# Kernel tuning notes

Hardware: AMD Instinct MI355X
Metric: run time of the kernel (lower is better)

## Reference

```python
import jax, jax.numpy as jnp
import numpy as np

ALPHA, GAMMA = 0.25, 2.0
ACCEPT, REJECT = 0.5, 0.4
CLF_W, REG_W = 1.0, 50.0
SL1_R = 9.0  # reg_smooth_l1_loss_scaling_factor
EPS = 1e-4


def _calc_iou(a, b):
    # a: [A,4] anchors in yxyx ; b: [M,4] gt boxes in xyxy (as in original code)
    ay1, ax1, ay2, ax2 = a[:, 0], a[:, 1], a[:, 2], a[:, 3]
    bx1, by1, bx2, by2 = b[:, 0], b[:, 1], b[:, 2], b[:, 3]
    iw = jnp.clip(jnp.minimum(ax2[:, None], bx2) - jnp.maximum(ax1[:, None], bx1), 0.0)
    ih = jnp.clip(jnp.minimum(ay2[:, None], by2) - jnp.maximum(ay1[:, None], by1), 0.0)
    inter = iw * ih  # [A, M]
    aarea = ((ax2 - ax1) * (ay2 - ay1))[:, None]
    barea = (bx2 - bx1) * (by2 - by1)
    union = jnp.clip(aarea + barea - inter, 1e-8)
    return inter / union


def _single_image(clf, reg, ann, anchors, a_cx, a_cy, a_w, a_h):
    # clf: [A,C], reg: [A,4], ann: [M,5] (x1,y1,x2,y2,label; label=-1 => pad)
    clf = jnp.clip(clf, EPS, 1.0 - EPS)
    labels = ann[:, 4]
    valid = labels != -1.0  # [M]
    boxes = ann[:, :4]
    iou = _calc_iou(anchors, boxes)               # [A, M]
    iou = jnp.where(valid[None, :], iou, -1.0)    # invalid GT never matches
    iou_max = iou.max(axis=-1)                    # [A]
    iou_arg = iou.argmax(axis=-1)                 # [A]
    matched = iou_max > ACCEPT
    unmatched = iou_max < REJECT
    num_matched = matched.sum()
    # classification targets: -1 (ignore) by default, 0 for unmatched, one-hot for matched
    gt_lbl = labels[iou_arg].astype(jnp.int32) - 1  # [A]
    one_hot = jax.nn.one_hot(gt_lbl, clf.shape[-1], dtype=clf.dtype)
    tgt = jnp.where(matched[:, None], one_hot,
                    jnp.where(unmatched[:, None], 0.0, -1.0))
    pos = ALPHA * (1.0 - clf) ** GAMMA * (-jnp.log(clf))
    neg = (1.0 - ALPHA) * clf ** GAMMA * (-jnp.log(1.0 - clf))
    clf_losses = jnp.where(tgt == 1.0, pos, neg)
    clf_losses = jnp.where(tgt == -1.0, 0.0, clf_losses)
    clf_loss = clf_losses.sum() / jnp.maximum(1, num_matched).astype(clf.dtype)
    gb = boxes[iou_arg]  # [A,4] xyxy
    gw_raw = gb[:, 2] - gb[:, 0]
    gh_raw = gb[:, 3] - gb[:, 1]
    gcx = gb[:, 0] + 0.5 * gw_raw
    gcy = gb[:, 1] + 0.5 * gh_raw
    gw = jnp.clip(gw_raw, 1.0)
    gh = jnp.clip(gh_raw, 1.0)
    reg_t = jnp.stack(((gcy - a_cy) / a_h,
                       (gcx - a_cx) / a_w,
                       jnp.log(gh / a_h),
                       jnp.log(gw / a_w)), axis=-1)  # [A,4] (dy,dx,dh,dw)
    d = jnp.abs(SL1_R * (reg - reg_t))
    sl1 = jnp.where(d < 1.0, 0.5 * d * d, d - 0.5)
    sl1 = jnp.where(matched[:, None], sl1, 0.0)
    denom = jnp.maximum(1, 4 * num_matched).astype(clf.dtype)
    reg_loss = jnp.where(num_matched > 0, sl1.sum() / denom, 0.0)
    return clf_loss, reg_loss


def setup_inputs() -> dict:
    key = jax.random.key(0)
    ks = jax.random.split(key, 12)
    B, A, C, M = 8, 49104, 90, 32
    clf = jax.random.uniform(ks[0], (B, A, C), jnp.float32)
    reg = jax.random.normal(ks[1], (B, A, 4), jnp.float32)
    # anchors in yxyx, all with positive width/height
    y1 = jax.random.uniform(ks[2], (A,)) * 480.0
    x1 = jax.random.uniform(ks[3], (A,)) * 480.0
    ah = jax.random.uniform(ks[4], (A,)) * 120.0 + 8.0
    aw = jax.random.uniform(ks[5], (A,)) * 120.0 + 8.0
    anchors = jnp.stack([y1, x1, y1 + ah, x1 + aw], axis=-1)[None].astype(jnp.float32)
    # annotations: xyxy boxes + label in [1, C]; ~half padded with label -1
    bx1 = jax.random.uniform(ks[6], (B, M)) * 400.0
    by1 = jax.random.uniform(ks[7], (B, M)) * 400.0
    bw = jax.random.uniform(ks[8], (B, M)) * 100.0 + 20.0
    bh = jax.random.uniform(ks[9], (B, M)) * 100.0 + 20.0
    lbl = jax.random.randint(ks[10], (B, M), 1, C + 1).astype(jnp.float32)
    lbl = jnp.where(jax.random.uniform(ks[11], (B, M)) < 0.6, lbl, -1.0)
    ann = jnp.stack([bx1, by1, bx1 + bw, by1 + bh, lbl], axis=-1).astype(jnp.float32)
    return {"classifications": clf, "regressions": reg, "anchors": anchors, "annotations": ann}


def reference(classifications, regressions, anchors, annotations):
    anc = anchors.squeeze()  # [A,4] yxyx
    a_w = anc[:, 3] - anc[:, 1]
    a_h = anc[:, 2] - anc[:, 0]
    a_cx = anc[:, 1] + 0.5 * a_w
    a_cy = anc[:, 0] + 0.5 * a_h
    clf = jnp.clip(classifications, EPS, 1.0 - EPS)
    clf_l, reg_l = jax.vmap(_single_image, in_axes=(0, 0, 0, None, None, None, None, None))(
        clf, regressions, annotations, anc, a_cx, a_cy, a_w, a_h)
    return CLF_W * clf_l.mean(), REG_W * reg_l.mean()
```

## Files before the change

kernel.cpp:

```cpp
#include <hip/hip_runtime.h>


namespace {
constexpr int B_N = 8;
constexpr int A_N = 49104;
constexpr int C_N = 90;
constexpr int M_N = 32;
constexpr float EPSF   = 1e-4f;
constexpr float ACCEPT = 0.5f;
constexpr float REJECT = 0.4f;
constexpr float SL1R   = 9.0f;
constexpr float CLFW   = 1.0f;
constexpr float REGW   = 50.0f;
constexpr float LN2    = 0.69314718055994530942f;

constexpr int MATCH_BX = 192;
constexpr int BASE_BX  = 256;

constexpr int BASEP_OFF  = 0;
constexpr int MATCHP_OFF = 2048;

__device__ __forceinline__ float clampx(float x) {
    return __builtin_amdgcn_fmed3f(x, EPSF, 1.0f - EPSF);
}
__device__ __forceinline__ float neg_term(float x) {
    x = clampx(x);
    return 0.75f * x * x * (-__logf(1.0f - x));
}
__device__ __forceinline__ float pos_term(float x) {
    x = clampx(x);
    float o = 1.0f - x;
    return 0.25f * o * o * (-__logf(x));
}
}

__global__ void match_kernel(const float* __restrict__ anchors,
                             const float* __restrict__ reg,
                             const float* __restrict__ ann,
                             const float* __restrict__ clf,
                             float* __restrict__ ws)
{
    __shared__ float sann[M_N * 5];
    __shared__ float sred[4][3];
    const int b   = blockIdx.y;
    const int tid = threadIdx.x;
    if (tid < M_N * 5) sann[tid] = ann[b * M_N * 5 + tid];
    __syncthreads();

    const int i = blockIdx.x * blockDim.x + tid;
    float cnt  = 0.0f;
    float rsum = 0.0f;
    float corr = 0.0f;

    if (i < A_N) {
        const float4 av = ((const float4*)anchors)[i];
        const float ay1 = av.x, ax1 = av.y, ay2 = av.z, ax2 = av.w;
        const float aw = ax2 - ax1, ah = ay2 - ay1;
        const float aarea = aw * ah;

        float best = -3.4e38f;
        int   arg  = 0;
        #pragma unroll 8
        for (int j = 0; j < M_N; ++j) {
            const float bx1 = sann[j*5+0], by1 = sann[j*5+1];
            const float bx2 = sann[j*5+2], by2 = sann[j*5+3];
            const float lb  = sann[j*5+4];
            float iw = fminf(ax2, bx2) - fmaxf(ax1, bx1); iw = fmaxf(iw, 0.0f);
            float ih = fminf(ay2, by2) - fmaxf(ay1, by1); ih = fmaxf(ih, 0.0f);
            const float inter = iw * ih;
            const float barea = (bx2 - bx1) * (by2 - by1);
            const float uni   = fmaxf(aarea + barea - inter, 1e-8f);
            float iou = inter / uni;
            if (lb == -1.0f) iou = -1.0f;
            if (iou > best) { best = iou; arg = j; }
        }

        const bool matched   = best > ACCEPT;
        const bool unmatched = best < REJECT;
        const float* __restrict__ row = clf + (size_t)(b * A_N + i) * C_N;

        if (matched) {
            const int s = (int)sann[arg*5+4] - 1;
            cnt = 1.0f;
            const float x = row[s];
            corr += pos_term(x) - neg_term(x);
            const float bx1 = sann[arg*5+0], by1 = sann[arg*5+1];
            const float bx2 = sann[arg*5+2], by2 = sann[arg*5+3];
            const float gwr = bx2 - bx1, ghr = by2 - by1;
            const float gcx = bx1 + 0.5f * gwr, gcy = by1 + 0.5f * ghr;
            const float gw  = fmaxf(gwr, 1.0f), gh = fmaxf(ghr, 1.0f);
            const float acx = ax1 + 0.5f * aw, acy = ay1 + 0.5f * ah;
            const float t0 = (gcy - acy) / ah;
            const float t1 = (gcx - acx) / aw;
            const float t2 = __logf(gh / ah);
            const float t3 = __logf(gw / aw);
            const float4 rv = ((const float4*)reg)[b * A_N + i];
            float d;
            d = fabsf(SL1R * (rv.x - t0)); rsum += (d < 1.0f) ? 0.5f*d*d : d - 0.5f;
            d = fabsf(SL1R * (rv.y - t1)); rsum += (d < 1.0f) ? 0.5f*d*d : d - 0.5f;
            d = fabsf(SL1R * (rv.z - t2)); rsum += (d < 1.0f) ? 0.5f*d*d : d - 0.5f;
            d = fabsf(SL1R * (rv.w - t3)); rsum += (d < 1.0f) ? 0.5f*d*d : d - 0.5f;
        } else if (!unmatched) {
            const float2* __restrict__ r2 = (const float2*)row;
            float rs = 0.0f;
            #pragma unroll
            for (int c = 0; c < C_N / 2; ++c) {
                const float2 u = r2[c];
                rs += neg_term(u.x) + neg_term(u.y);
            }
            corr -= rs;
        }
    }

    #pragma unroll
    for (int off = 32; off > 0; off >>= 1) {
        cnt  += __shfl_down(cnt,  off);
        rsum += __shfl_down(rsum, off);
        corr += __shfl_down(corr, off);
    }
    const int wid = tid >> 6;
    if ((tid & 63) == 0) {
        sred[wid][0] = cnt; sred[wid][1] = rsum; sred[wid][2] = corr;
    }
    __syncthreads();
    if (tid == 0) {
        float c = 0.f, r = 0.f, k = 0.f;
        #pragma unroll
        for (int w = 0; w < 4; ++w) { c += sred[w][0]; r += sred[w][1]; k += sred[w][2]; }
        float4* mp = (float4*)(ws + MATCHP_OFF);
        mp[b * MATCH_BX + blockIdx.x] = make_float4(c, r, k, 0.0f);
    }
}

__global__ void base_kernel(const float* __restrict__ clf,
                            float*       __restrict__ ws)
{
    constexpr unsigned TOT_F4 = (unsigned)(A_N * C_N) / 4u;
    constexpr unsigned Q      = TOT_F4 / 4u;
    const int b = blockIdx.y;
    const float4* __restrict__ p = (const float4*)(clf + (size_t)b * A_N * C_N);

    float sum = 0.0f;
    const unsigned stride = gridDim.x * blockDim.x;

    auto work4 = [](float4 v) -> float {
        float s = 0.0f;
        float x0 = clampx(v.x), x1 = clampx(v.y), x2 = clampx(v.z), x3 = clampx(v.w);
        s = fmaf(x0 * x0, __log2f(1.0f - x0), s);
        s = fmaf(x1 * x1, __log2f(1.0f - x1), s);
        s = fmaf(x2 * x2, __log2f(1.0f - x2), s);
        s = fmaf(x3 * x3, __log2f(1.0f - x3), s);
        return s;
    };

    for (unsigned f = blockIdx.x * blockDim.x + threadIdx.x; f < Q; f += stride) {
        const float4 v0 = p[f];
        const float4 v1 = p[f + Q];
        const float4 v2 = p[f + 2u * Q];
        const float4 v3 = p[f + 3u * Q];
        sum += work4(v0) + work4(v1) + work4(v2) + work4(v3);
    }

    __shared__ float sred[4];
    #pragma unroll
    for (int off = 32; off > 0; off >>= 1) sum += __shfl_down(sum, off);
    const int tid = threadIdx.x;
    if ((tid & 63) == 0) sred[tid >> 6] = sum;
    __syncthreads();
    if (tid == 0) {
        ws[BASEP_OFF + b * BASE_BX + blockIdx.x] =
            sred[0] + sred[1] + sred[2] + sred[3];
    }
}

__global__ void finalize_kernel(const float* __restrict__ ws,
                                float*       __restrict__ out)
{
    __shared__ float s_base[B_N], s_cnt[B_N], s_rsum[B_N], s_corr[B_N];
    const int tid = threadIdx.x;
    const int b   = tid >> 5;
    const int j   = tid & 31;

    float base = 0.f, cnt = 0.f, rsum = 0.f, corr = 0.f;
    #pragma unroll
    for (int k = 0; k < BASE_BX / 32; ++k)
        base += ws[BASEP_OFF + b * BASE_BX + j + 32 * k];
    const float4* mp = (const float4*)(ws + MATCHP_OFF);
    #pragma unroll
    for (int k = 0; k < MATCH_BX / 32; ++k) {
        const float4 m = mp[b * MATCH_BX + j + 32 * k];
        cnt += m.x; rsum += m.y; corr += m.z;
    }
    #pragma unroll
    for (int off = 16; off > 0; off >>= 1) {
        base += __shfl_down(base, off, 32);
        cnt  += __shfl_down(cnt,  off, 32);
        rsum += __shfl_down(rsum, off, 32);
        corr += __shfl_down(corr, off, 32);
    }
    if (j == 0) { s_base[b] = base; s_cnt[b] = cnt; s_rsum[b] = rsum; s_corr[b] = corr; }
    __syncthreads();
    if (tid == 0) {
        float cl = 0.0f, rl = 0.0f;
        #pragma unroll
        for (int bb = 0; bb < B_N; ++bb) {
            const float n = s_cnt[bb];
            const float clf_total = -0.75f * LN2 * s_base[bb] + s_corr[bb];
            cl += clf_total / fmaxf(1.0f, n);
            if (n > 0.0f) rl += s_rsum[bb] / (4.0f * n);
        }
        out[0] = CLFW * (cl / (float)B_N);
        out[1] = REGW * (rl / (float)B_N);
    }
}

extern "C" void kernel_launch(void* const* d_in, const int* in_sizes, int n_in,
                              void* d_out, int out_size, void* d_ws, size_t ws_size,
                              hipStream_t stream) {
    const float* clf     = (const float*)d_in[0];
    const float* reg     = (const float*)d_in[1];
    const float* anchors = (const float*)d_in[2];
    const float* ann     = (const float*)d_in[3];
    float* out = (float*)d_out;
    float* ws  = (float*)d_ws;

    {
        dim3 grid(MATCH_BX, B_N);
        match_kernel<<<grid, 256, 0, stream>>>(anchors, reg, ann, clf, ws);
    }
    {
        dim3 grid(BASE_BX, B_N);
        base_kernel<<<grid, 256, 0, stream>>>(clf, ws);
    }
    finalize_kernel<<<1, 256, 0, stream>>>(ws, out);
}
```

Measured before the change: 238.6 us.

## Fuse anchor matching and focal-loss streaming into one per-tile kernel

```diff
diff --git a/kernel.cpp b/kernel.cpp
--- a/kernel.cpp
+++ b/kernel.cpp
@@ -12,45 +12,35 @@
 constexpr float SL1R   = 9.0f;
 constexpr float CLFW   = 1.0f;
 constexpr float REGW   = 50.0f;
-constexpr float LN2    = 0.69314718055994530942f;
 
-constexpr int MATCH_BX = 192;
-constexpr int BASE_BX  = 256;
-
-constexpr int BASEP_OFF  = 0;
-constexpr int MATCHP_OFF = 2048;
+constexpr int APB     = 256;
+constexpr int NBX     = (A_N + APB - 1) / APB;
 
 __device__ __forceinline__ float clampx(float x) {
     return __builtin_amdgcn_fmed3f(x, EPSF, 1.0f - EPSF);
 }
-__device__ __forceinline__ float neg_term(float x) {
-    x = clampx(x);
-    return 0.75f * x * x * (-__logf(1.0f - x));
-}
-__device__ __forceinline__ float pos_term(float x) {
-    x = clampx(x);
-    float o = 1.0f - x;
-    return 0.25f * o * o * (-__logf(x));
-}
 }
 
-__global__ void match_kernel(const float* __restrict__ anchors,
+__global__ void fused_kernel(const float* __restrict__ anchors,
                              const float* __restrict__ reg,
                              const float* __restrict__ ann,
                              const float* __restrict__ clf,
-                             float* __restrict__ ws)
+                             float4* __restrict__ part)
 {
     __shared__ float sann[M_N * 5];
+    __shared__ int   sstate[APB];
     __shared__ float sred[4][3];
+
     const int b   = blockIdx.y;
+    const int a0  = blockIdx.x * APB;
     const int tid = threadIdx.x;
     if (tid < M_N * 5) sann[tid] = ann[b * M_N * 5 + tid];
     __syncthreads();
 
-    const int i = blockIdx.x * blockDim.x + tid;
     float cnt  = 0.0f;
     float rsum = 0.0f;
-    float corr = 0.0f;
+    int   s    = -2;
+    const int i = a0 + tid;
 
     if (i < A_N) {
         const float4 av = ((const float4*)anchors)[i];
@@ -77,13 +67,10 @@
 
         const bool matched   = best > ACCEPT;
         const bool unmatched = best < REJECT;
-        const float* __restrict__ row = clf + (size_t)(b * A_N + i) * C_N;
 
         if (matched) {
-            const int s = (int)sann[arg*5+4] - 1;
+            s   = (int)sann[arg*5+4] - 1;
             cnt = 1.0f;
-            const float x = row[s];
-            corr += pos_term(x) - neg_term(x);
             const float bx1 = sann[arg*5+0], by1 = sann[arg*5+1];
             const float bx2 = sann[arg*5+2], by2 = sann[arg*5+3];
             const float gwr = bx2 - bx1, ghr = by2 - by1;
@@ -100,113 +87,93 @@
             d = fabsf(SL1R * (rv.y - t1)); rsum += (d < 1.0f) ? 0.5f*d*d : d - 0.5f;
             d = fabsf(SL1R * (rv.z - t2)); rsum += (d < 1.0f) ? 0.5f*d*d : d - 0.5f;
             d = fabsf(SL1R * (rv.w - t3)); rsum += (d < 1.0f) ? 0.5f*d*d : d - 0.5f;
-        } else if (!unmatched) {
-            const float2* __restrict__ r2 = (const float2*)row;
-            float rs = 0.0f;
-            #pragma unroll
-            for (int c = 0; c < C_N / 2; ++c) {
-                const float2 u = r2[c];
-                rs += neg_term(u.x) + neg_term(u.y);
-            }
-            corr -= rs;
+        } else {
+            s = unmatched ? -1 : -2;
         }
+    }
+    sstate[tid] = s;
+    __syncthreads();
+
+    const int nA  = min(APB, A_N - a0);
+    const int nF4 = nA * C_N / 4;
+    const float4* __restrict__ p =
+        (const float4*)(clf + ((size_t)b * A_N + a0) * C_N);
+
+    float csum = 0.0f;
+
+    auto term = [&](float x, int st, int c) -> float {
+        const bool ispos = (st == c);
+        x = clampx(x);
+        const float y  = ispos ? x : 1.0f - x;
+        float al = ispos ? -0.25f : -0.75f;
+        al = (st == -2) ? 0.0f : al;
+        const float o = 1.0f - y;
+        return al * o * o * __logf(y);
+    };
+
+    for (int f = tid; f < nF4; f += 256) {
+        const float4 v = p[f];
+        const int idx = 4 * f;
+        const int a   = (int)((unsigned)idx / 90u);
+        const int c0  = idx - 90 * a;
+        const bool strad = (c0 == 88);
+        const int s0 = sstate[a];
+        const int s1 = strad ? sstate[a + 1] : s0;
+        const int c2 = strad ? 0 : c0 + 2;
+        const int c3 = strad ? 1 : c0 + 3;
+        csum += term(v.x, s0, c0);
+        csum += term(v.y, s0, c0 + 1);
+        csum += term(v.z, s1, c2);
+        csum += term(v.w, s1, c3);
     }
 
     #pragma unroll
     for (int off = 32; off > 0; off >>= 1) {
         cnt  += __shfl_down(cnt,  off);
         rsum += __shfl_down(rsum, off);
-        corr += __shfl_down(corr, off);
+        csum += __shfl_down(csum, off);
     }
     const int wid = tid >> 6;
     if ((tid & 63) == 0) {
-        sred[wid][0] = cnt; sred[wid][1] = rsum; sred[wid][2] = corr;
+        sred[wid][0] = cnt; sred[wid][1] = rsum; sred[wid][2] = csum;
     }
     __syncthreads();
     if (tid == 0) {
         float c = 0.f, r = 0.f, k = 0.f;
         #pragma unroll
         for (int w = 0; w < 4; ++w) { c += sred[w][0]; r += sred[w][1]; k += sred[w][2]; }
-        float4* mp = (float4*)(ws + MATCHP_OFF);
-        mp[b * MATCH_BX + blockIdx.x] = make_float4(c, r, k, 0.0f);
+        part[b * NBX + blockIdx.x] = make_float4(c, r, k, 0.0f);
     }
 }
 
-__global__ void base_kernel(const float* __restrict__ clf,
-                            float*       __restrict__ ws)
+__global__ void finalize_kernel(const float4* __restrict__ part,
+                                float*        __restrict__ out)
 {
-    constexpr unsigned TOT_F4 = (unsigned)(A_N * C_N) / 4u;
-    constexpr unsigned Q      = TOT_F4 / 4u;
-    const int b = blockIdx.y;
-    const float4* __restrict__ p = (const float4*)(clf + (size_t)b * A_N * C_N);
-
-    float sum = 0.0f;
-    const unsigned stride = gridDim.x * blockDim.x;
-
-    auto work4 = [](float4 v) -> float {
-        float s = 0.0f;
-        float x0 = clampx(v.x), x1 = clampx(v.y), x2 = clampx(v.z), x3 = clampx(v.w);
-        s = fmaf(x0 * x0, __log2f(1.0f - x0), s);
-        s = fmaf(x1 * x1, __log2f(1.0f - x1), s);
-        s = fmaf(x2 * x2, __log2f(1.0f - x2), s);
-        s = fmaf(x3 * x3, __log2f(1.0f - x3), s);
-        return s;
-    };
-
-    for (unsigned f = blockIdx.x * blockDim.x + threadIdx.x; f < Q; f += stride) {
-        const float4 v0 = p[f];
-        const float4 v1 = p[f + Q];
-        const float4 v2 = p[f + 2u * Q];
-        const float4 v3 = p[f + 3u * Q];
-        sum += work4(v0) + work4(v1) + work4(v2) + work4(v3);
-    }
-
-    __shared__ float sred[4];
-    #pragma unroll
-    for (int off = 32; off > 0; off >>= 1) sum += __shfl_down(sum, off);
-    const int tid = threadIdx.x;
-    if ((tid & 63) == 0) sred[tid >> 6] = sum;
-    __syncthreads();
-    if (tid == 0) {
-        ws[BASEP_OFF + b * BASE_BX + blockIdx.x] =
-            sred[0] + sred[1] + sred[2] + sred[3];
-    }
-}
-
-__global__ void finalize_kernel(const float* __restrict__ ws,
-                                float*       __restrict__ out)
-{
-    __shared__ float s_base[B_N], s_cnt[B_N], s_rsum[B_N], s_corr[B_N];
+    __shared__ float s_cnt[B_N], s_rsum[B_N], s_csum[B_N];
     const int tid = threadIdx.x;
     const int b   = tid >> 5;
     const int j   = tid & 31;
 
-    float base = 0.f, cnt = 0.f, rsum = 0.f, corr = 0.f;
+    float cnt = 0.f, rsum = 0.f, csum = 0.f;
     #pragma unroll
-    for (int k = 0; k < BASE_BX / 32; ++k)
-        base += ws[BASEP_OFF + b * BASE_BX + j + 32 * k];
-    const float4* mp = (const float4*)(ws + MATCHP_OFF);
-    #pragma unroll
-    for (int k = 0; k < MATCH_BX / 32; ++k) {
-        const float4 m = mp[b * MATCH_BX + j + 32 * k];
-        cnt += m.x; rsum += m.y; corr += m.z;
+    for (int k = 0; k < NBX / 32; ++k) {
+        const float4 m = part[b * NBX + j + 32 * k];
+        cnt += m.x; rsum += m.y; csum += m.z;
     }
     #pragma unroll
     for (int off = 16; off > 0; off >>= 1) {
-        base += __shfl_down(base, off, 32);
         cnt  += __shfl_down(cnt,  off, 32);
         rsum += __shfl_down(rsum, off, 32);
-        corr += __shfl_down(corr, off, 32);
+        csum += __shfl_down(csum, off, 32);
     }
-    if (j == 0) { s_base[b] = base; s_cnt[b] = cnt; s_rsum[b] = rsum; s_corr[b] = corr; }
+    if (j == 0) { s_cnt[b] = cnt; s_rsum[b] = rsum; s_csum[b] = csum; }
     __syncthreads();
     if (tid == 0) {
         float cl = 0.0f, rl = 0.0f;
         #pragma unroll
         for (int bb = 0; bb < B_N; ++bb) {
             const float n = s_cnt[bb];
-            const float clf_total = -0.75f * LN2 * s_base[bb] + s_corr[bb];
-            cl += clf_total / fmaxf(1.0f, n);
+            cl += s_csum[bb] / fmaxf(1.0f, n);
             if (n > 0.0f) rl += s_rsum[bb] / (4.0f * n);
         }
         out[0] = CLFW * (cl / (float)B_N);
@@ -221,16 +188,12 @@
     const float* reg     = (const float*)d_in[1];
     const float* anchors = (const float*)d_in[2];
     const float* ann     = (const float*)d_in[3];
-    float* out = (float*)d_out;
-    float* ws  = (float*)d_ws;
+    float*  out  = (float*)d_out;
+    float4* part = (float4*)d_ws;
 
     {
-        dim3 grid(MATCH_BX, B_N);
-        match_kernel<<<grid, 256, 0, stream>>>(anchors, reg, ann, clf, ws);
+        dim3 grid(NBX, B_N);
+        fused_kernel<<<grid, 256, 0, stream>>>(anchors, reg, ann, clf, part);
     }
-    {
-        dim3 grid(BASE_BX, B_N);
-        base_kernel<<<grid, 256, 0, stream>>>(clf, ws);
-    }
-    finalize_kernel<<<1, 256, 0, stream>>>(ws, out);
+    finalize_kernel<<<1, 256, 0, stream>>>(part, out);
 }
```

Result: faster. 218.3 us (-8.5%).
